# Optimization experiments

Hardware: AMD Instinct MI355X
Metric: run time of the kernel (lower is better)

Reference implementation:

```python
import jax, jax.numpy as jnp
import numpy as np

N = 100000      # nodes (single node type)
R = 4           # relations
E = 800000      # edges per relation (avg in-degree ~32)
D_IN, D_H, D_OUT = 256, 64, 16


def setup_inputs() -> dict:
    key = jax.random.key(0)
    ks = jax.random.split(key, 9)
    x = jax.random.normal(ks[0], (N, D_IN), dtype=jnp.float32)
    src = jax.random.randint(ks[1], (R, E), 0, N, dtype=jnp.int32)
    dst = jax.random.randint(ks[2], (R, E), 0, N, dtype=jnp.int32)
    s_in = 1.0 / np.sqrt(D_IN)
    s_h = 1.0 / np.sqrt(D_H)
    W1 = jax.random.normal(ks[3], (R, D_IN, D_H), dtype=jnp.float32) * s_in
    L1w = jax.random.normal(ks[4], (D_IN, D_H), dtype=jnp.float32) * s_in
    L1b = jnp.zeros((D_H,), dtype=jnp.float32)
    W2 = jax.random.normal(ks[5], (R, D_H, D_OUT), dtype=jnp.float32) * s_h
    L2w = jax.random.normal(ks[6], (D_H, D_OUT), dtype=jnp.float32) * s_h
    L2b = jnp.zeros((D_OUT,), dtype=jnp.float32)
    return {"x": x, "src": src, "dst": dst, "W1": W1, "L1w": L1w,
            "L1b": L1b, "W2": W2, "L2w": L2w, "L2b": L2b}


def _rel_graph_conv(h, src, dst, W):
    """Per-relation GEMM + gather + scatter-add + right-normalize, summed over relations.
    h: [N, d_in]; src/dst: [R, E]; W: [R, d_in, d_out] -> [N, d_out]
    """
    hw = jnp.einsum('nd,rdh->rnh', h, W)  # transform first (d_out small), then gather

    def agg(hr, s, d):
        deg = jax.ops.segment_sum(jnp.ones((E,), hr.dtype), d, num_segments=N)
        msg = jax.ops.segment_sum(hr[s], d, num_segments=N)  # [N, d_out]
        return msg / jnp.maximum(deg, 1.0)[:, None]          # norm='right'

    return jnp.sum(jax.vmap(agg)(hw, src, dst), axis=0)


def reference(x, src, dst, W1, L1w, L1b, W2, L2w, L2b):
    # Layer 1: relation conv + self-loop linear + ReLU (dropout = eval/identity)
    h = _rel_graph_conv(x, src, dst, W1) + x @ L1w + L1b
    h = jax.nn.relu(h)
    # Layer 2: no activation
    out = _rel_graph_conv(h, src, dst, W2) + h @ L2w + L2b
    return out
```

## Files before the change

### kernel.cpp

```cpp
#include <hip/hip_runtime.h>


constexpr int NN = 100000, RR = 4, EE = 800000;
constexpr int RE = RR * EE;
constexpr int NBKT = (NN + 63) / 64;
constexpr int BCAP = 3072;
constexpr int NG1 = (NN + 63) / 64;
constexpr int CHUNK = 8192;
constexpr int NB = (RE + CHUNK - 1) / CHUNK;
constexpr int EPT = CHUNK / 512;

typedef short bf16x8 __attribute__((ext_vector_type(8)));
typedef float f32x4 __attribute__((ext_vector_type(4)));

__device__ inline unsigned short f2bf(float f) {
  unsigned u = __float_as_uint(f);
  u += 0x7FFF + ((u >> 16) & 1);
  return (unsigned short)(u >> 16);
}
__device__ inline float bf2f(unsigned short s) {
  return __uint_as_float(((unsigned)s) << 16);
}

__global__ __launch_bounds__(256) void prep_w_kernel(const float* __restrict__ W1,
                                                     const float* __restrict__ L1w,
                                                     const float* __restrict__ W2,
                                                     const float* __restrict__ L2w,
                                                     unsigned short* __restrict__ BT1,
                                                     unsigned short* __restrict__ BT2) {
  int idx = blockIdx.x * 256 + threadIdx.x;
  if (idx < 320 * 256) {
    int n = idx >> 8, k = idx & 255;
    float v = (n < 256) ? W1[((size_t)((n >> 6) * 256 + k)) * 64 + (n & 63)]
                        : L1w[(size_t)k * 64 + (n - 256)];
    BT1[idx] = f2bf(v);
  } else {
    int j = idx - 320 * 256;
    if (j < 80 * 64) {
      int n = j >> 6, k = j & 63;
      float v = (n < 64) ? W2[((size_t)((n >> 4) * 64 + k)) * 16 + (n & 15)]
                         : L2w[(size_t)k * 16 + (n - 64)];
      BT2[j] = f2bf(v);
    }
  }
}

__global__ __launch_bounds__(512) void fused1_kernel(const float* __restrict__ x,
                                                     const unsigned short* __restrict__ BT1,
                                                     const float* __restrict__ L1b,
                                                     const int* __restrict__ src,
                                                     const int* __restrict__ dst,
                                                     int* __restrict__ gcur,
                                                     int* __restrict__ binned,
                                                     unsigned short* __restrict__ hwcat,
                                                     unsigned short* __restrict__ h) {
  __shared__ char lds[49152];
  const int bid = blockIdx.x;
  const int t = threadIdx.x;
  const bool is_bin = (bid % 5 == 0) && (bid / 5 < NB);

  if (is_bin) {
    int* hist = (int*)lds;
    int* base = hist + NBKT;
    for (int k = t; k < NBKT; k += 512) hist[k] = 0;
    __syncthreads();
    const int e0 = (bid / 5) * CHUNK + t;
    int dl[EPT], sl[EPT];
#pragma unroll
    for (int i = 0; i < EPT; ++i) {
      int fl = e0 + i * 512;
      dl[i] = -1;
      if (fl < RE) {
        dl[i] = dst[fl];
        sl[i] = src[fl];
        atomicAdd(&hist[dl[i] >> 6], 1);
      }
    }
    __syncthreads();
    for (int k = t; k < NBKT; k += 512) {
      int hv = hist[k];
      base[k] = hv ? atomicAdd(&gcur[k], hv) : 0;
      hist[k] = 0;
    }
    __syncthreads();
#pragma unroll
    for (int i = 0; i < EPT; ++i) {
      if (dl[i] < 0) continue;
      int fl = e0 + i * 512;
      int r = fl / EE;
      int b = dl[i] >> 6;
      int off = atomicAdd(&hist[b], 1);
      int p = base[b] + off;
      if (p < BCAP) binned[(size_t)b * BCAP + p] = sl[i] | (r << 17) | ((dl[i] & 63) << 19);
    }
    return;
  }

  int nbins = (bid + 4) / 5;
  if (nbins > NB) nbins = NB;
  const int m0 = (bid - nbins) * 64;
  char* Al = lds;
  char* Bl = lds + 64 * 64 * 2;
  const int wid = t >> 6, lane = t & 63;
  const int wm = wid >> 2, wn = wid & 3;
  const int l15 = lane & 15, g = lane >> 4;

  f32x4 acc[2][5];
#pragma unroll
  for (int i = 0; i < 2; ++i)
#pragma unroll
    for (int j = 0; j < 5; ++j) acc[i][j] = (f32x4){0.f, 0.f, 0.f, 0.f};

  for (int kc = 0; kc < 4; ++kc) {
    if (kc) __syncthreads();
#pragma unroll
    for (int it = 0; it < 2; ++it) {
      int fl = t + 512 * it;
      int row = fl >> 4, kq = (fl & 15) * 4;
      int rg = m0 + row;
      float4 v = (rg < NN) ? *(const float4*)(x + (size_t)rg * 256 + kc * 64 + kq)
                           : make_float4(0.f, 0.f, 0.f, 0.f);
      ushort4 pck = {f2bf(v.x), f2bf(v.y), f2bf(v.z), f2bf(v.w)};
      int wb = ((row * 64 + kq) * 2) ^ ((row & 7) << 4);
      *(ushort4*)(Al + wb) = pck;
    }
#pragma unroll
    for (int it = 0; it < 5; ++it) {
      int fl = t + 512 * it;
      int n = fl >> 3, i8 = (fl & 7) * 8;
      uint4 u = *(const uint4*)(BT1 + (size_t)n * 256 + kc * 64 + i8);
      int wb = ((n * 64 + i8) * 2) ^ ((n & 7) << 4);
      *(uint4*)(Bl + wb) = u;
    }
    __syncthreads();
#pragma unroll
    for (int ks = 0; ks < 2; ++ks) {
      bf16x8 af[2], bfr[5];
#pragma unroll
      for (int mi = 0; mi < 2; ++mi) {
        int row = wm * 32 + mi * 16 + l15;
        int byte = ((row * 64 + ks * 32 + g * 8) * 2) ^ ((row & 7) << 4);
        af[mi] = *(const bf16x8*)(Al + byte);
      }
#pragma unroll
      for (int ni = 0; ni < 5; ++ni) {
        int n = wn * 80 + ni * 16 + l15;
        int byte = ((n * 64 + ks * 32 + g * 8) * 2) ^ ((n & 7) << 4);
        bfr[ni] = *(const bf16x8*)(Bl + byte);
      }
#pragma unroll
      for (int mi = 0; mi < 2; ++mi)
#pragma unroll
        for (int ni = 0; ni < 5; ++ni)
          acc[mi][ni] = __builtin_amdgcn_mfma_f32_16x16x32_bf16(af[mi], bfr[ni], acc[mi][ni], 0, 0, 0);
    }
  }
#pragma unroll
  for (int mi = 0; mi < 2; ++mi) {
    int rbase = m0 + wm * 32 + mi * 16 + 4 * g;
#pragma unroll
    for (int ni = 0; ni < 5; ++ni) {
      int n0 = wn * 80 + ni * 16;
      int n = n0 + l15;
#pragma unroll
      for (int e = 0; e < 4; ++e) {
        int row = rbase + e;
        if (row >= NN) continue;
        float v = acc[mi][ni][e];
        if (n0 < 256) hwcat[(size_t)row * 256 + n] = f2bf(v);
        else h[(size_t)row * 64 + (n - 256)] = f2bf(v + L1b[n - 256]);
      }
    }
  }
}

__global__ __launch_bounds__(256) void pull1_kernel(const unsigned short* __restrict__ h,
                                                    const unsigned short* __restrict__ hwcat,
                                                    const int* __restrict__ binned,
                                                    const int* __restrict__ gcur,
                                                    const unsigned short* __restrict__ BT2,
                                                    const float* __restrict__ L2b,
                                                    unsigned short* __restrict__ hw2,
                                                    float* __restrict__ out) {
  __shared__ int csr[BCAP];
  __shared__ int cnt[256];
  __shared__ int off[256];
  __shared__ int deg[256];
  __shared__ float htile[64][64];
  const int t = threadIdx.x, bkt = blockIdx.x;
  const int wid = t >> 6, lane = t & 63;
  const int l15 = lane & 15, g = lane >> 4;

  int count = gcur[bkt];
  if (count > BCAP) count = BCAP;
  const int* edges = binned + (size_t)bkt * BCAP;

  cnt[t] = 0;
  __syncthreads();
  for (int i = t; i < count; i += 256) {
    int w = edges[i];
    atomicAdd(&cnt[((w >> 19) & 63) * 4 + ((w >> 17) & 3)], 1);
  }
  __syncthreads();
  off[t] = cnt[t];
  __syncthreads();
  for (int s = 1; s < 256; s <<= 1) {
    int v = (t >= s) ? off[t - s] : 0;
    __syncthreads();
    off[t] += v;
    __syncthreads();
  }
  int excl = off[t] - cnt[t];
  deg[t] = cnt[t];
  __syncthreads();
  off[t] = excl;
  cnt[t] = excl;
  __syncthreads();
  for (int i = t; i < count; i += 256) {
    int w = edges[i];
    int k = ((w >> 19) & 63) * 4 + ((w >> 17) & 3);
    int p = atomicAdd(&cnt[k], 1);
    csr[p] = w & 0x1FFFF;
  }
  __syncthreads();

  const int slot = lane >> 3, cpart = lane & 7;
  for (int ii = 0; ii < 16; ++ii) {
    int nloc = wid * 16 + ii;
    float acc[8] = {0.f, 0.f, 0.f, 0.f, 0.f, 0.f, 0.f, 0.f};
#pragma unroll
    for (int r = 0; r < 4; ++r) {
      int k = nloc * 4 + r;
      int beg = off[k], dg = deg[k];
      float w = 1.0f / (float)(dg > 1 ? dg : 1);
      for (int p0 = 0; p0 < dg; p0 += 8) {
        int j = p0 + slot;
        bool pr = j < dg;
        int s = pr ? csr[beg + j] : 0;
        uint4 u = *(const uint4*)(hwcat + (size_t)s * 256 + r * 64 + cpart * 8);
        float wp = pr ? w : 0.f;
#pragma unroll
        for (int q = 0; q < 4; ++q) {
          unsigned uu = (&u.x)[q];
          acc[q * 2]     = fmaf(wp, bf2f((unsigned short)(uu & 0xffffu)), acc[q * 2]);
          acc[q * 2 + 1] = fmaf(wp, bf2f((unsigned short)(uu >> 16)), acc[q * 2 + 1]);
        }
      }
    }
#pragma unroll
    for (int m = 8; m <= 32; m <<= 1)
#pragma unroll
      for (int q = 0; q < 8; ++q) acc[q] += __shfl_xor(acc[q], m);
    if (slot == 0) {
      *(float4*)&htile[nloc][cpart * 8]     = make_float4(acc[0], acc[1], acc[2], acc[3]);
      *(float4*)&htile[nloc][cpart * 8 + 4] = make_float4(acc[4], acc[5], acc[6], acc[7]);
    }
  }
  __syncthreads();

  const int row = t >> 2, c0 = (t & 3) * 16;
  const int gn = bkt * 64 + row;
  float vals[16];
#pragma unroll
  for (int q = 0; q < 16; ++q) vals[q] = htile[row][c0 + q];
  if (gn < NN) {
    uint4 h0 = *(const uint4*)(h + (size_t)gn * 64 + c0);
    uint4 h1 = *(const uint4*)(h + (size_t)gn * 64 + c0 + 8);
#pragma unroll
    for (int q = 0; q < 4; ++q) {
      unsigned a = (&h0.x)[q], b = (&h1.x)[q];
      vals[q * 2]     += bf2f((unsigned short)(a & 0xffffu));
      vals[q * 2 + 1] += bf2f((unsigned short)(a >> 16));
      vals[8 + q * 2]     += bf2f((unsigned short)(b & 0xffffu));
      vals[8 + q * 2 + 1] += bf2f((unsigned short)(b >> 16));
    }
  }
  unsigned pk[8];
#pragma unroll
  for (int q = 0; q < 8; ++q) {
    float v0 = fmaxf(vals[q * 2], 0.f), v1 = fmaxf(vals[q * 2 + 1], 0.f);
    pk[q] = (unsigned)f2bf(v0) | ((unsigned)f2bf(v1) << 16);
  }
  __syncthreads();

  char* Al = (char*)htile;
  {
    int wb = ((row * 64 + c0) * 2) ^ ((row & 7) << 4);
    *(uint4*)(Al + wb) = make_uint4(pk[0], pk[1], pk[2], pk[3]);
    int wb2 = ((row * 64 + c0 + 8) * 2) ^ ((row & 7) << 4);
    *(uint4*)(Al + wb2) = make_uint4(pk[4], pk[5], pk[6], pk[7]);
  }
  char* Bl = (char*)csr;
#pragma unroll
  for (int it = 0; it < 3; ++it) {
    int fl = t + 256 * it;
    if (fl < 640) {
      int n = fl >> 3, i8 = (fl & 7) * 8;
      uint4 u = *(const uint4*)(BT2 + (size_t)n * 64 + i8);
      int wb = ((n * 64 + i8) * 2) ^ ((n & 7) << 4);
      *(uint4*)(Bl + wb) = u;
    }
  }
  __syncthreads();

  f32x4 acc2[5];
#pragma unroll
  for (int j = 0; j < 5; ++j) acc2[j] = (f32x4){0.f, 0.f, 0.f, 0.f};
#pragma unroll
  for (int ks = 0; ks < 2; ++ks) {
    int ra = wid * 16 + l15;
    int byte = ((ra * 64 + ks * 32 + g * 8) * 2) ^ ((ra & 7) << 4);
    bf16x8 af = *(const bf16x8*)(Al + byte);
#pragma unroll
    for (int ni = 0; ni < 5; ++ni) {
      int n = ni * 16 + l15;
      int nb = ((n * 64 + ks * 32 + g * 8) * 2) ^ ((n & 7) << 4);
      bf16x8 bfr = *(const bf16x8*)(Bl + nb);
      acc2[ni] = __builtin_amdgcn_mfma_f32_16x16x32_bf16(af, bfr, acc2[ni], 0, 0, 0);
    }
  }
  int rb = wid * 16 + 4 * g;
#pragma unroll
  for (int ni = 0; ni < 5; ++ni) {
    int n0 = ni * 16;
    int n = n0 + l15;
#pragma unroll
    for (int e = 0; e < 4; ++e) {
      int gno = bkt * 64 + rb + e;
      if (gno >= NN) continue;
      float vv = acc2[ni][e];
      if (n0 < 64) hw2[(size_t)gno * 64 + n] = f2bf(vv);
      else out[(size_t)gno * 16 + (n - 64)] = vv + L2b[n - 64];
    }
  }
}

__global__ __launch_bounds__(256) void pull2_kernel(const unsigned short* __restrict__ hw2,
                                                    const int* __restrict__ binned,
                                                    const int* __restrict__ gcur,
                                                    float* __restrict__ out) {
  __shared__ int csr[BCAP];
  __shared__ int cnt[256];
  __shared__ int off[256];
  __shared__ int deg[256];
  __shared__ float ot[64][16];
  const int t = threadIdx.x, bkt = blockIdx.x;
  const int wid = t >> 6, lane = t & 63;

  int count = gcur[bkt];
  if (count > BCAP) count = BCAP;
  const int* edges = binned + (size_t)bkt * BCAP;

  cnt[t] = 0;
  __syncthreads();
  for (int i = t; i < count; i += 256) {
    int w = edges[i];
    atomicAdd(&cnt[((w >> 19) & 63) * 4 + ((w >> 17) & 3)], 1);
  }
  __syncthreads();
  off[t] = cnt[t];
  __syncthreads();
  for (int s = 1; s < 256; s <<= 1) {
    int v = (t >= s) ? off[t - s] : 0;
    __syncthreads();
    off[t] += v;
    __syncthreads();
  }
  int excl = off[t] - cnt[t];
  deg[t] = cnt[t];
  __syncthreads();
  off[t] = excl;
  cnt[t] = excl;
  __syncthreads();
  for (int i = t; i < count; i += 256) {
    int w = edges[i];
    int k = ((w >> 19) & 63) * 4 + ((w >> 17) & 3);
    int p = atomicAdd(&cnt[k], 1);
    csr[p] = w & 0x1FFFF;
  }
  __syncthreads();

  const int slot = lane >> 2, cpart = lane & 3;
  for (int ii = 0; ii < 16; ++ii) {
    int nloc = wid * 16 + ii;
    float acc[4] = {0.f, 0.f, 0.f, 0.f};
#pragma unroll
    for (int r = 0; r < 4; ++r) {
      int k = nloc * 4 + r;
      int beg = off[k], dg = deg[k];
      float w = 1.0f / (float)(dg > 1 ? dg : 1);
      for (int p0 = 0; p0 < dg; p0 += 16) {
        int j = p0 + slot;
        bool pr = j < dg;
        int s = pr ? csr[beg + j] : 0;
        uint2 u = *(const uint2*)(hw2 + (size_t)s * 64 + r * 16 + cpart * 4);
        float wp = pr ? w : 0.f;
        acc[0] = fmaf(wp, bf2f((unsigned short)(u.x & 0xffffu)), acc[0]);
        acc[1] = fmaf(wp, bf2f((unsigned short)(u.x >> 16)), acc[1]);
        acc[2] = fmaf(wp, bf2f((unsigned short)(u.y & 0xffffu)), acc[2]);
        acc[3] = fmaf(wp, bf2f((unsigned short)(u.y >> 16)), acc[3]);
      }
    }
#pragma unroll
    for (int m = 4; m <= 32; m <<= 1)
#pragma unroll
      for (int q = 0; q < 4; ++q) acc[q] += __shfl_xor(acc[q], m);
    if (slot == 0)
      *(float4*)&ot[nloc][cpart * 4] = make_float4(acc[0], acc[1], acc[2], acc[3]);
  }
  __syncthreads();

  int row = t >> 2, q = t & 3;
  int gn = bkt * 64 + row;
  if (gn < NN) {
    float4 o = *(float4*)(out + (size_t)gn * 16 + q * 4);
    float4 a = *(float4*)&ot[row][q * 4];
    o.x += a.x; o.y += a.y; o.z += a.z; o.w += a.w;
    *(float4*)(out + (size_t)gn * 16 + q * 4) = o;
  }
}

extern "C" void kernel_launch(void* const* d_in, const int* in_sizes, int n_in,
                              void* d_out, int out_size, void* d_ws, size_t ws_size,
                              hipStream_t stream) {
  const float* x   = (const float*)d_in[0];
  const int*   src = (const int*)d_in[1];
  const int*   dst = (const int*)d_in[2];
  const float* W1  = (const float*)d_in[3];
  const float* L1w = (const float*)d_in[4];
  const float* L1b = (const float*)d_in[5];
  const float* W2  = (const float*)d_in[6];
  const float* L2w = (const float*)d_in[7];
  const float* L2b = (const float*)d_in[8];
  float* out = (float*)d_out;

  char* p = (char*)d_ws;
  int* binned = (int*)p;                      p += (size_t)NBKT * BCAP * 4;
  int* gcur   = (int*)p;                      p += 8192;
  unsigned short* hwcat = (unsigned short*)p; p += (size_t)NN * 256 * 2;
  unsigned short* h = (unsigned short*)p;     p += (size_t)NN * 64 * 2;
  unsigned short* hw2 = (unsigned short*)p;   p += (size_t)NN * 64 * 2;
  unsigned short* BT1 = (unsigned short*)p;   p += 320 * 256 * 2;
  unsigned short* BT2 = (unsigned short*)p;   p += 80 * 64 * 2;
  if ((size_t)(p - (char*)d_ws) > ws_size) return;

  hipMemsetAsync(gcur, 0, NBKT * 4, stream);
  prep_w_kernel<<<(320 * 256 + 80 * 64 + 255) / 256, 256, 0, stream>>>(W1, L1w, W2, L2w, BT1, BT2);
  fused1_kernel<<<NG1 + NB, 512, 0, stream>>>(x, BT1, L1b, src, dst, gcur, binned, hwcat, h);
  pull1_kernel<<<NBKT, 256, 0, stream>>>(h, hwcat, binned, gcur, BT2, L2b, hw2, out);
  pull2_kernel<<<NBKT, 256, 0, stream>>>(hw2, binned, gcur, out);
}
```

Baseline: 263.6 us.

## Merge per-relation edge loops into one loop and fuse residual/ReLU into reduction

Edge keys are re-encoded as (src<<2)|rel, so the key directly indexes the row-plus-relation slice of hwcat/hw2. The four per-relation inner loops collapse into one loop over all of a node's edges, with a per-(node,relation) inverse degree looked up from shared memory. This cuts partial-wave waste from four separate tails down to one. In pull1 the self-loop add, ReLU and bf16 packing now happen right after the shuffle reduction by the slot-0 lanes, dropping the fp32 htile round trip and one barrier. The costs are an extra LDS lookup per edge and the bf16 epilogue being done by fewer lanes.

After: 229.7 us. -12.9%, faster.

```diff
diff --git a/kernel.cpp b/kernel.cpp
--- a/kernel.cpp
+++ b/kernel.cpp
@@ -91,7 +91,7 @@
       int b = dl[i] >> 6;
       int off = atomicAdd(&hist[b], 1);
       int p = base[b] + off;
-      if (p < BCAP) binned[(size_t)b * BCAP + p] = sl[i] | (r << 17) | ((dl[i] & 63) << 19);
+      if (p < BCAP) binned[(size_t)b * BCAP + p] = (sl[i] << 2) | r | ((dl[i] & 63) << 19);
     }
     return;
   }
@@ -185,8 +185,9 @@
   __shared__ int csr[BCAP];
   __shared__ int cnt[256];
   __shared__ int off[256];
-  __shared__ int deg[256];
-  __shared__ float htile[64][64];
+  __shared__ float winv[256];
+  __shared__ int tot[64];
+  __shared__ char Al[64 * 64 * 2];
   const int t = threadIdx.x, bkt = blockIdx.x;
   const int wid = t >> 6, lane = t & 63;
   const int l15 = lane & 15, g = lane >> 4;
@@ -199,7 +200,7 @@
   __syncthreads();
   for (int i = t; i < count; i += 256) {
     int w = edges[i];
-    atomicAdd(&cnt[((w >> 19) & 63) * 4 + ((w >> 17) & 3)], 1);
+    atomicAdd(&cnt[((w >> 19) & 63) * 4 + (w & 3)], 1);
   }
   __syncthreads();
   off[t] = cnt[t];
@@ -211,40 +212,38 @@
     __syncthreads();
   }
   int excl = off[t] - cnt[t];
-  deg[t] = cnt[t];
+  winv[t] = 1.0f / (float)(cnt[t] > 1 ? cnt[t] : 1);
   __syncthreads();
   off[t] = excl;
   cnt[t] = excl;
   __syncthreads();
+  if (t < 64) tot[t] = ((t == 63) ? count : off[(t + 1) * 4]) - off[t * 4];
+  __syncthreads();
   for (int i = t; i < count; i += 256) {
     int w = edges[i];
-    int k = ((w >> 19) & 63) * 4 + ((w >> 17) & 3);
+    int k = ((w >> 19) & 63) * 4 + (w & 3);
     int p = atomicAdd(&cnt[k], 1);
-    csr[p] = w & 0x1FFFF;
+    csr[p] = w & 0x7FFFF;
   }
   __syncthreads();
 
   const int slot = lane >> 3, cpart = lane & 7;
   for (int ii = 0; ii < 16; ++ii) {
     int nloc = wid * 16 + ii;
+    int beg = off[nloc * 4];
+    int total = tot[nloc];
     float acc[8] = {0.f, 0.f, 0.f, 0.f, 0.f, 0.f, 0.f, 0.f};
-#pragma unroll
-    for (int r = 0; r < 4; ++r) {
-      int k = nloc * 4 + r;
-      int beg = off[k], dg = deg[k];
-      float w = 1.0f / (float)(dg > 1 ? dg : 1);
-      for (int p0 = 0; p0 < dg; p0 += 8) {
-        int j = p0 + slot;
-        bool pr = j < dg;
-        int s = pr ? csr[beg + j] : 0;
-        uint4 u = *(const uint4*)(hwcat + (size_t)s * 256 + r * 64 + cpart * 8);
-        float wp = pr ? w : 0.f;
-#pragma unroll
-        for (int q = 0; q < 4; ++q) {
-          unsigned uu = (&u.x)[q];
-          acc[q * 2]     = fmaf(wp, bf2f((unsigned short)(uu & 0xffffu)), acc[q * 2]);
-          acc[q * 2 + 1] = fmaf(wp, bf2f((unsigned short)(uu >> 16)), acc[q * 2 + 1]);
-        }
+    for (int p0 = 0; p0 < total; p0 += 8) {
+      int j = p0 + slot;
+      bool pr = j < total;
+      int key = pr ? csr[beg + j] : 0;
+      float wv = pr ? winv[nloc * 4 + (key & 3)] : 0.f;
+      uint4 u = *(const uint4*)(hwcat + (size_t)key * 64 + cpart * 8);
+#pragma unroll
+      for (int q = 0; q < 4; ++q) {
+        unsigned uu = (&u.x)[q];
+        acc[q * 2]     = fmaf(wv, bf2f((unsigned short)(uu & 0xffffu)), acc[q * 2]);
+        acc[q * 2 + 1] = fmaf(wv, bf2f((unsigned short)(uu >> 16)), acc[q * 2 + 1]);
       }
     }
 #pragma unroll
@@ -252,44 +251,23 @@
 #pragma unroll
       for (int q = 0; q < 8; ++q) acc[q] += __shfl_xor(acc[q], m);
     if (slot == 0) {
-      *(float4*)&htile[nloc][cpart * 8]     = make_float4(acc[0], acc[1], acc[2], acc[3]);
-      *(float4*)&htile[nloc][cpart * 8 + 4] = make_float4(acc[4], acc[5], acc[6], acc[7]);
-    }
-  }
-  __syncthreads();
-
-  const int row = t >> 2, c0 = (t & 3) * 16;
-  const int gn = bkt * 64 + row;
-  float vals[16];
-#pragma unroll
-  for (int q = 0; q < 16; ++q) vals[q] = htile[row][c0 + q];
-  if (gn < NN) {
-    uint4 h0 = *(const uint4*)(h + (size_t)gn * 64 + c0);
-    uint4 h1 = *(const uint4*)(h + (size_t)gn * 64 + c0 + 8);
-#pragma unroll
-    for (int q = 0; q < 4; ++q) {
-      unsigned a = (&h0.x)[q], b = (&h1.x)[q];
-      vals[q * 2]     += bf2f((unsigned short)(a & 0xffffu));
-      vals[q * 2 + 1] += bf2f((unsigned short)(a >> 16));
-      vals[8 + q * 2]     += bf2f((unsigned short)(b & 0xffffu));
-      vals[8 + q * 2 + 1] += bf2f((unsigned short)(b >> 16));
-    }
-  }
-  unsigned pk[8];
-#pragma unroll
-  for (int q = 0; q < 8; ++q) {
-    float v0 = fmaxf(vals[q * 2], 0.f), v1 = fmaxf(vals[q * 2 + 1], 0.f);
-    pk[q] = (unsigned)f2bf(v0) | ((unsigned)f2bf(v1) << 16);
-  }
-  __syncthreads();
-
-  char* Al = (char*)htile;
-  {
-    int wb = ((row * 64 + c0) * 2) ^ ((row & 7) << 4);
-    *(uint4*)(Al + wb) = make_uint4(pk[0], pk[1], pk[2], pk[3]);
-    int wb2 = ((row * 64 + c0 + 8) * 2) ^ ((row & 7) << 4);
-    *(uint4*)(Al + wb2) = make_uint4(pk[4], pk[5], pk[6], pk[7]);
-  }
+      int gn = bkt * 64 + nloc;
+      unsigned pk[4];
+      uint4 hu = make_uint4(0, 0, 0, 0);
+      if (gn < NN) hu = *(const uint4*)(h + (size_t)gn * 64 + cpart * 8);
+#pragma unroll
+      for (int q = 0; q < 4; ++q) {
+        unsigned a = (&hu.x)[q];
+        float v0 = acc[q * 2]     + bf2f((unsigned short)(a & 0xffffu));
+        float v1 = acc[q * 2 + 1] + bf2f((unsigned short)(a >> 16));
+        pk[q] = (unsigned)f2bf(fmaxf(v0, 0.f)) | ((unsigned)f2bf(fmaxf(v1, 0.f)) << 16);
+      }
+      int wb = ((nloc * 64 + cpart * 8) * 2) ^ ((nloc & 7) << 4);
+      *(uint4*)(Al + wb) = make_uint4(pk[0], pk[1], pk[2], pk[3]);
+    }
+  }
+  __syncthreads();
+
   char* Bl = (char*)csr;
 #pragma unroll
   for (int it = 0; it < 3; ++it) {
@@ -342,7 +320,8 @@
   __shared__ int csr[BCAP];
   __shared__ int cnt[256];
   __shared__ int off[256];
-  __shared__ int deg[256];
+  __shared__ float winv[256];
+  __shared__ int tot[64];
   __shared__ float ot[64][16];
   const int t = threadIdx.x, bkt = blockIdx.x;
   const int wid = t >> 6, lane = t & 63;
@@ -355,7 +334,7 @@
   __syncthreads();
   for (int i = t; i < count; i += 256) {
     int w = edges[i];
-    atomicAdd(&cnt[((w >> 19) & 63) * 4 + ((w >> 17) & 3)], 1);
+    atomicAdd(&cnt[((w >> 19) & 63) * 4 + (w & 3)], 1);
   }
   __syncthreads();
   off[t] = cnt[t];
@@ -367,39 +346,37 @@
     __syncthreads();
   }
   int excl = off[t] - cnt[t];
-  deg[t] = cnt[t];
+  winv[t] = 1.0f / (float)(cnt[t] > 1 ? cnt[t] : 1);
   __syncthreads();
   off[t] = excl;
   cnt[t] = excl;
   __syncthreads();
+  if (t < 64) tot[t] = ((t == 63) ? count : off[(t + 1) * 4]) - off[t * 4];
+  __syncthreads();
   for (int i = t; i < count; i += 256) {
     int w = edges[i];
-    int k = ((w >> 19) & 63) * 4 + ((w >> 17) & 3);
+    int k = ((w >> 19) & 63) * 4 + (w & 3);
     int p = atomicAdd(&cnt[k], 1);
-    csr[p] = w & 0x1FFFF;
+    csr[p] = w & 0x7FFFF;
   }
   __syncthreads();
 
   const int slot = lane >> 2, cpart = lane & 3;
   for (int ii = 0; ii < 16; ++ii) {
     int nloc = wid * 16 + ii;
+    int beg = off[nloc * 4];
+    int total = tot[nloc];
     float acc[4] = {0.f, 0.f, 0.f, 0.f};
-#pragma unroll
-    for (int r = 0; r < 4; ++r) {
-      int k = nloc * 4 + r;
-      int beg = off[k], dg = deg[k];
-      float w = 1.0f / (float)(dg > 1 ? dg : 1);
-      for (int p0 = 0; p0 < dg; p0 += 16) {
-        int j = p0 + slot;
-        bool pr = j < dg;
-        int s = pr ? csr[beg + j] : 0;
-        uint2 u = *(const uint2*)(hw2 + (size_t)s * 64 + r * 16 + cpart * 4);
-        float wp = pr ? w : 0.f;
-        acc[0] = fmaf(wp, bf2f((unsigned short)(u.x & 0xffffu)), acc[0]);
-        acc[1] = fmaf(wp, bf2f((unsigned short)(u.x >> 16)), acc[1]);
-        acc[2] = fmaf(wp, bf2f((unsigned short)(u.y & 0xffffu)), acc[2]);
-        acc[3] = fmaf(wp, bf2f((unsigned short)(u.y >> 16)), acc[3]);
-      }
+    for (int p0 = 0; p0 < total; p0 += 16) {
+      int j = p0 + slot;
+      bool pr = j < total;
+      int key = pr ? csr[beg + j] : 0;
+      float wv = pr ? winv[nloc * 4 + (key & 3)] : 0.f;
+      uint2 u = *(const uint2*)(hw2 + (size_t)key * 16 + cpart * 4);
+      acc[0] = fmaf(wv, bf2f((unsigned short)(u.x & 0xffffu)), acc[0]);
+      acc[1] = fmaf(wv, bf2f((unsigned short)(u.x >> 16)), acc[1]);
+      acc[2] = fmaf(wv, bf2f((unsigned short)(u.y & 0xffffu)), acc[2]);
+      acc[3] = fmaf(wv, bf2f((unsigned short)(u.y >> 16)), acc[3]);
     }
 #pragma unroll
     for (int m = 4; m <= 32; m <<= 1)
```
